# Optimization experiments

Hardware: AMD Instinct MI355X
Metric: run time of the kernel (lower is better)

Reference implementation:

```python
import jax, jax.numpy as jnp
import numpy as np

B, L, D = 8, 2048, 1024   # batch, seq_len, d_model
E, H, K = 8, 512, 2       # num_experts, expert_hidden, top_k
LN_EPS = 1e-5


def setup_inputs() -> dict:
    key = jax.random.key(0)
    ks = jax.random.split(key, 4)
    rn = lambda k, shape, sc: (jax.random.normal(k, shape, jnp.float32) * sc)
    return {
        "x": rn(ks[0], (B, L, D), 1.0),
        "ln_w": jnp.ones((D,), jnp.float32),
        "ln_b": jnp.zeros((D,), jnp.float32),
        "gate_w": rn(ks[1], (D, E), 0.02),
        "gate_b": jnp.zeros((E,), jnp.float32),
        "w1": rn(ks[2], (E, D, H), 0.02),
        "b1": jnp.zeros((E, H), jnp.float32),
        "w2": rn(ks[3], (E, H, D), 0.02),
        "b2": jnp.zeros((E, D), jnp.float32),
    }


def reference(x, ln_w, ln_b, gate_w, gate_b, w1, b1, w2, b2):
    Bx, Lx, Dx = x.shape
    xf = x.reshape(-1, Dx)                                   # [N, D]

    # gate = LayerNorm -> Linear (eval mode: no noise)
    mu = xf.mean(-1, keepdims=True)
    var = ((xf - mu) ** 2).mean(-1, keepdims=True)
    xn = (xf - mu) * jax.lax.rsqrt(var + LN_EPS) * ln_w + ln_b
    gate_logits = xn @ gate_w + gate_b                       # [N, E]
    gate_weights = jax.nn.softmax(gate_logits, axis=-1)      # [N, E]

    top_w, top_idx = jax.lax.top_k(gate_weights, K)          # [N, K]
    top_w = top_w / top_w.sum(-1, keepdims=True)

    # dense all-experts compute (faithful to the torch module)
    h = jax.nn.gelu(jnp.einsum('nd,edh->neh', xf, w1) + b1, approximate=False)  # [N, E, H]
    expert_out = jnp.einsum('neh,ehd->ned', h, w2) + b2      # [N, E, D]

    # gather selected experts and weighted-combine
    sel = jnp.take_along_axis(expert_out, top_idx[:, :, None], axis=1)  # [N, K, D]
    out = (top_w[:, :, None] * sel).sum(axis=1).reshape(Bx, Lx, Dx)
    return out, gate_weights
```

## Files before the change

kernel.cpp:

```cpp
#include <hip/hip_runtime.h>
#include <hip/hip_bf16.h>

#define N_TOK 16384
#define DM 1024
#define HD 512
#define NE 8
#define LN_EPS 1e-5f

typedef __attribute__((ext_vector_type(8))) short v8s;
typedef __attribute__((ext_vector_type(4))) float v4f;

__device__ __forceinline__ unsigned short f2bf(float f) {
  union { float f; unsigned u; } c; c.f = f;
  unsigned u = c.u + 0x7FFFu + ((c.u >> 16) & 1u);
  return (unsigned short)(u >> 16);
}

__device__ __forceinline__ float gelu_f(float v) {
  return 0.5f * v * (1.0f + erff(v * 0.7071067811865475f));
}

__global__ __launch_bounds__(256) void gate_kernel(
    const float* __restrict__ x, const float* __restrict__ lnw,
    const float* __restrict__ lnb, const float* __restrict__ gw,
    const float* __restrict__ gb, float* __restrict__ gates_out,
    int* __restrict__ ce, float* __restrict__ cw)
{
  const int wv = threadIdx.x >> 6, l = threadIdx.x & 63;
  const int n = blockIdx.x * 4 + wv;
  const float* xr = x + (size_t)n * DM;
  float4 v[4]; float s = 0.f, s2 = 0.f;
#pragma unroll
  for (int j = 0; j < 4; ++j) {
    v[j] = *(const float4*)(xr + l * 4 + j * 256);
    s  += v[j].x + v[j].y + v[j].z + v[j].w;
    s2 += v[j].x * v[j].x + v[j].y * v[j].y + v[j].z * v[j].z + v[j].w * v[j].w;
  }
#pragma unroll
  for (int m = 1; m < 64; m <<= 1) { s += __shfl_xor(s, m); s2 += __shfl_xor(s2, m); }
  const float mu = s * (1.f / DM);
  const float var = s2 * (1.f / DM) - mu * mu;
  const float rstd = 1.f / sqrtf(var + LN_EPS);
  float acc[8] = {0, 0, 0, 0, 0, 0, 0, 0};
#pragma unroll
  for (int j = 0; j < 4; ++j) {
#pragma unroll
    for (int q = 0; q < 4; ++q) {
      int d = l * 4 + j * 256 + q;
      float xv = (q == 0) ? v[j].x : (q == 1) ? v[j].y : (q == 2) ? v[j].z : v[j].w;
      float xn = (xv - mu) * rstd * lnw[d] + lnb[d];
      const float4 g0 = *(const float4*)(gw + d * 8);
      const float4 g1 = *(const float4*)(gw + d * 8 + 4);
      acc[0] += xn * g0.x; acc[1] += xn * g0.y; acc[2] += xn * g0.z; acc[3] += xn * g0.w;
      acc[4] += xn * g1.x; acc[5] += xn * g1.y; acc[6] += xn * g1.z; acc[7] += xn * g1.w;
    }
  }
#pragma unroll
  for (int e = 0; e < 8; ++e)
#pragma unroll
    for (int m = 1; m < 64; m <<= 1) acc[e] += __shfl_xor(acc[e], m);

  if (l == 0) {
    float lg[8], p[8], g[8];
    float mx = -1e30f;
    for (int e = 0; e < 8; ++e) { lg[e] = acc[e] + gb[e]; mx = fmaxf(mx, lg[e]); }
    float sum = 0.f;
    for (int e = 0; e < 8; ++e) { p[e] = expf(lg[e] - mx); sum += p[e]; }
    float inv = 1.f / sum;
    for (int e = 0; e < 8; ++e) g[e] = p[e] * inv;
    float4* go = (float4*)(gates_out + (size_t)n * 8);
    go[0] = make_float4(g[0], g[1], g[2], g[3]);
    go[1] = make_float4(g[4], g[5], g[6], g[7]);
    int e0 = 0; float b0 = g[0];
    for (int e = 1; e < 8; ++e) if (g[e] > b0) { b0 = g[e]; e0 = e; }
    int e1 = -1; float b1v = -1.f;
    for (int e = 0; e < 8; ++e) if (e != e0 && g[e] > b1v) { b1v = g[e]; e1 = e; }
    float wsum = b0 + b1v;
    ce[2 * n] = e0; ce[2 * n + 1] = e1;
    cw[2 * n] = b0 / wsum; cw[2 * n + 1] = b1v / wsum;
  }
}

__global__ __launch_bounds__(256) void route_kernel(
    const int* __restrict__ ce, const float* __restrict__ cw,
    int* __restrict__ counts, int* __restrict__ tids, float* __restrict__ pws)
{
  __shared__ int cnt;
  const int e = blockIdx.x;
  if (threadIdx.x == 0) cnt = 0;
  __syncthreads();
  for (int i = threadIdx.x; i < 2 * N_TOK; i += 256) {
    if (ce[i] == e) {
      int p = atomicAdd(&cnt, 1);
      tids[e * N_TOK + p] = i >> 1;
      pws[e * N_TOK + p] = cw[i];
    }
  }
  __syncthreads();
  if (threadIdx.x == 0) counts[e] = cnt;
}

__global__ __launch_bounds__(256) void transpose_cvt(
    const float* __restrict__ in, unsigned short* __restrict__ out, int R, int C)
{
  __shared__ float tile[64][65];
  const int tilesC = C >> 6, tilesR = R >> 6;
  const int perE = tilesR * tilesC;
  int bt = blockIdx.x;
  const int e = bt / perE; int rem = bt - e * perE;
  const int tr = rem / tilesC, tc = rem - tr * tilesC;
  const float* ip = in + (size_t)e * R * C;
  unsigned short* op = out + (size_t)e * R * C;
  const int r0 = tr * 64, c0 = tc * 64;
#pragma unroll
  for (int i = 0; i < 16; ++i) {
    int idx = i * 256 + threadIdx.x;
    int rr = idx >> 6, cc = idx & 63;
    tile[rr][cc] = ip[(size_t)(r0 + rr) * C + (c0 + cc)];
  }
  __syncthreads();
#pragma unroll
  for (int i = 0; i < 16; ++i) {
    int idx = i * 256 + threadIdx.x;
    int rr = idx >> 6, cc = idx & 63;
    op[(size_t)(c0 + rr) * R + (r0 + cc)] = f2bf(tile[cc][rr]);
  }
}

#define H_OFF   0
#define XS_OFF  65536
#define W1S_OFF 73728
#define W2S_OFF 65536
#define TOK_OFF 139264
#define WT_OFF  139520
#define SMEM_BYTES 139776

template<bool FULL>
__global__ __launch_bounds__(512, 2) void ffn_kernel(
    const float* __restrict__ x,
    const float* __restrict__ w1, const float* __restrict__ b1,
    const float* __restrict__ w2, const float* __restrict__ b2,
    const unsigned short* __restrict__ w1t, const unsigned short* __restrict__ w2t,
    const int* __restrict__ counts, const int* __restrict__ tids,
    const float* __restrict__ pws, float* __restrict__ outp)
{
  extern __shared__ char smem[];
  const int e = blockIdx.x & 7;
  const int tile = blockIdx.x >> 3;
  const int cnt = counts[e];
  const int base = tile * 64;
  if (base >= cnt) return;
  const int t = threadIdx.x;
  const int w = t >> 6, l = t & 63;
  const int lrow = l & 15, lhi = l >> 4;

  int* tokL = (int*)(smem + TOK_OFF);
  float* wtL = (float*)(smem + WT_OFF);
  if (t < 64) {
    int i = base + t;
    bool ok = i < cnt;
    int src = e * N_TOK + (ok ? i : base);
    tokL[t] = tids[src];
    wtL[t] = ok ? pws[src] : 0.f;
  }
  __syncthreads();

  v4f acc[4][4];
#pragma unroll
  for (int a = 0; a < 4; ++a)
#pragma unroll
    for (int b = 0; b < 4; ++b) acc[a][b] = (v4f){0.f, 0.f, 0.f, 0.f};

  for (int kt = 0; kt < 16; ++kt) {
    const int k0 = kt * 64;
    {
      const int tokr = t >> 3, ks = t & 7;
      const float* src = x + (size_t)tokL[tokr] * DM + k0 + ks * 8;
      float f[8];
      *(float4*)(f) = *(const float4*)src;
      *(float4*)(f + 4) = *(const float4*)(src + 4);
      v8s pv;
#pragma unroll
      for (int j = 0; j < 8; ++j) pv[j] = (short)f2bf(f[j]);
      *(v8s*)(smem + XS_OFF + tokr * 128 + ((ks ^ (tokr & 7)) << 4)) = pv;
    }
    if (FULL) {
#pragma unroll
      for (int i = 0; i < 8; ++i) {
        int c = i * 512 + t;
        int h = c >> 3, ks = c & 7;
        v8s val = *(const v8s*)(w1t + ((size_t)e * HD + h) * DM + k0 + ks * 8);
        *(v8s*)(smem + W1S_OFF + h * 128 + ((ks ^ (h & 7)) << 4)) = val;
      }
    } else {
      const int h = t;
#pragma unroll
      for (int i = 0; i < 8; ++i) {
        float f[8];
#pragma unroll
        for (int j = 0; j < 8; ++j) f[j] = w1[((size_t)e * DM + k0 + i * 8 + j) * HD + h];
        v8s pv;
#pragma unroll
        for (int j = 0; j < 8; ++j) pv[j] = (short)f2bf(f[j]);
        *(v8s*)(smem + W1S_OFF + h * 128 + ((i ^ (h & 7)) << 4)) = pv;
      }
    }
    __syncthreads();
#pragma unroll
    for (int ks2 = 0; ks2 < 2; ++ks2) {
      const int sb = (ks2 << 2) + lhi;
      v8s af[4], bfr[4];
#pragma unroll
      for (int mi = 0; mi < 4; ++mi) {
        int row = mi * 16 + lrow;
        af[mi] = *(const v8s*)(smem + XS_OFF + row * 128 + ((sb ^ (row & 7)) << 4));
      }
#pragma unroll
      for (int nj = 0; nj < 4; ++nj) {
        int col = (w << 6) + nj * 16 + lrow;
        bfr[nj] = *(const v8s*)(smem + W1S_OFF + col * 128 + ((sb ^ (col & 7)) << 4));
      }
#pragma unroll
      for (int mi = 0; mi < 4; ++mi)
#pragma unroll
        for (int nj = 0; nj < 4; ++nj)
          acc[mi][nj] = __builtin_amdgcn_mfma_f32_16x16x32_bf16(af[mi], bfr[nj], acc[mi][nj], 0, 0, 0);
    }
    __syncthreads();
  }

#pragma unroll
  for (int nj = 0; nj < 4; ++nj) {
    const int col = (w << 6) + nj * 16 + lrow;
    const float b1v = b1[e * HD + col];
#pragma unroll
    for (int mi = 0; mi < 4; ++mi) {
#pragma unroll
      for (int r = 0; r < 4; ++r) {
        int row = mi * 16 + lhi * 4 + r;
        float g = gelu_f(acc[mi][nj][r] + b1v);
        *(unsigned short*)(smem + H_OFF + row * 1024 + ((col * 2) ^ ((row & 7) << 4))) = f2bf(g);
      }
    }
  }
  __syncthreads();

  for (int nc = 0; nc < 4; ++nc) {
    v4f acc2[4][2];
#pragma unroll
    for (int a = 0; a < 4; ++a)
#pragma unroll
      for (int b = 0; b < 2; ++b) acc2[a][b] = (v4f){0.f, 0.f, 0.f, 0.f};
    for (int k2 = 0; k2 < 8; ++k2) {
      const int h0 = k2 * 64;
      if (FULL) {
#pragma unroll
        for (int i = 0; i < 4; ++i) {
          int c = i * 512 + t;
          int dloc = c >> 3, ks = c & 7;
          v8s val = *(const v8s*)(w2t + ((size_t)e * DM + nc * 256 + dloc) * HD + h0 + ks * 8);
          *(v8s*)(smem + W2S_OFF + dloc * 128 + ((ks ^ (dloc & 7)) << 4)) = val;
        }
      } else {
        const int dloc = t & 255;
        const int kb = t >> 8;
#pragma unroll
        for (int i = 0; i < 4; ++i) {
          int ks = kb + i * 2;
          float f[8];
#pragma unroll
          for (int j = 0; j < 8; ++j) f[j] = w2[((size_t)e * HD + h0 + ks * 8 + j) * DM + nc * 256 + dloc];
          v8s pv;
#pragma unroll
          for (int j = 0; j < 8; ++j) pv[j] = (short)f2bf(f[j]);
          *(v8s*)(smem + W2S_OFF + dloc * 128 + ((ks ^ (dloc & 7)) << 4)) = pv;
        }
      }
      __syncthreads();
#pragma unroll
      for (int ks2 = 0; ks2 < 2; ++ks2) {
        const int sb = (ks2 << 2) + lhi;
        v8s af[4], bfr[2];
#pragma unroll
        for (int mi = 0; mi < 4; ++mi) {
          int row = mi * 16 + lrow;
          int slin = (h0 >> 3) + sb;
          af[mi] = *(const v8s*)(smem + H_OFF + row * 1024 + ((slin ^ (row & 7)) << 4));
        }
#pragma unroll
        for (int nj = 0; nj < 2; ++nj) {
          int dl = (w << 5) + nj * 16 + lrow;
          bfr[nj] = *(const v8s*)(smem + W2S_OFF + dl * 128 + ((sb ^ (dl & 7)) << 4));
        }
#pragma unroll
        for (int mi = 0; mi < 4; ++mi)
#pragma unroll
          for (int nj = 0; nj < 2; ++nj)
            acc2[mi][nj] = __builtin_amdgcn_mfma_f32_16x16x32_bf16(af[mi], bfr[nj], acc2[mi][nj], 0, 0, 0);
      }
      __syncthreads();
    }
#pragma unroll
    for (int nj = 0; nj < 2; ++nj) {
      const int dl = (w << 5) + nj * 16 + lrow;
      const int d = nc * 256 + dl;
      const float b2v = b2[e * DM + d];
#pragma unroll
      for (int mi = 0; mi < 4; ++mi) {
#pragma unroll
        for (int r = 0; r < 4; ++r) {
          int row = mi * 16 + lhi * 4 + r;
          float val = wtL[row] * (acc2[mi][nj][r] + b2v);
          atomicAdd(outp + (size_t)tokL[row] * DM + d, val);
        }
      }
    }
  }
}

extern "C" void kernel_launch(void* const* d_in, const int* in_sizes, int n_in,
                              void* d_out, int out_size, void* d_ws, size_t ws_size,
                              hipStream_t stream)
{
  const float* x   = (const float*)d_in[0];
  const float* lnw = (const float*)d_in[1];
  const float* lnb = (const float*)d_in[2];
  const float* gw  = (const float*)d_in[3];
  const float* gb  = (const float*)d_in[4];
  const float* w1  = (const float*)d_in[5];
  const float* b1  = (const float*)d_in[6];
  const float* w2  = (const float*)d_in[7];
  const float* b2  = (const float*)d_in[8];
  float* out = (float*)d_out;
  float* gates_out = out + (size_t)N_TOK * DM;

  char* ws = (char*)d_ws;
  int*   ce     = (int*)(ws + 0);
  float* cw     = (float*)(ws + 131072);
  int*   counts = (int*)(ws + 262144);
  int*   tids   = (int*)(ws + 262400);
  float* pws    = (float*)(ws + 786688);
  unsigned short* w1t = (unsigned short*)(ws + 1310976);
  unsigned short* w2t = (unsigned short*)(ws + 9699584);
  const bool full = ws_size >= 18088192ull;

  hipMemsetAsync(d_out, 0, (size_t)N_TOK * DM * sizeof(float), stream);
  gate_kernel<<<N_TOK / 4, 256, 0, stream>>>(x, lnw, lnb, gw, gb, gates_out, ce, cw);
  route_kernel<<<NE, 256, 0, stream>>>(ce, cw, counts, tids, pws);
  if (full) {
    transpose_cvt<<<NE * 16 * 8, 256, 0, stream>>>(w1, w1t, DM, HD);
    transpose_cvt<<<NE * 8 * 16, 256, 0, stream>>>(w2, w2t, HD, DM);
    hipFuncSetAttribute((const void*)&ffn_kernel<true>,
                        hipFuncAttributeMaxDynamicSharedMemorySize, SMEM_BYTES);
    ffn_kernel<true><<<NE * 256, 512, SMEM_BYTES, stream>>>(
        x, w1, b1, w2, b2, w1t, w2t, counts, tids, pws, out);
  } else {
    hipFuncSetAttribute((const void*)&ffn_kernel<false>,
                        hipFuncAttributeMaxDynamicSharedMemorySize, SMEM_BYTES);
    ffn_kernel<false><<<NE * 256, 512, SMEM_BYTES, stream>>>(
        x, w1, b1, w2, b2, w1t, w2t, counts, tids, pws, out);
  }
}
```

Measured before the change: 614.9 us.

## Split fused expert FFN into two grouped bf16 GEMMs with direct-to-LDS loads

When the workspace is large enough, the gate kernel also writes a bf16 copy of x. The fused per-expert FFN is replaced by two grouped GEMM kernels: gemm1 computes GELU(x W1 + b1) into a bf16 hidden buffer, and gemm2 multiplies by W2 and atomically accumulates the routing-weighted result into the output. Both use 128x128 tiles, swizzled LDS and global_load_lds transfers, and launch a fixed grid sized for the worst case, with surplus blocks exiting early. This targets better MFMA utilization and occupancy, at the cost of a hidden-state round trip through global memory, extra workspace, and fp32 atomics on the output.

```diff
diff --git a/kernel.cpp b/kernel.cpp
--- a/kernel.cpp
+++ b/kernel.cpp
@@ -6,9 +6,17 @@
 #define HD 512
 #define NE 8
 #define LN_EPS 1e-5f
+#define MT_MAX 264
 
 typedef __attribute__((ext_vector_type(8))) short v8s;
 typedef __attribute__((ext_vector_type(4))) float v4f;
+
+typedef const __attribute__((address_space(1))) unsigned int* as1cu;
+typedef __attribute__((address_space(3))) unsigned int* as3u;
+
+__device__ __forceinline__ void gl_lds16(const void* g, void* l) {
+  __builtin_amdgcn_global_load_lds((as1cu)g, (as3u)l, 16, 0, 0);
+}
 
 __device__ __forceinline__ unsigned short f2bf(float f) {
   union { float f; unsigned u; } c; c.f = f;
@@ -24,7 +32,8 @@
     const float* __restrict__ x, const float* __restrict__ lnw,
     const float* __restrict__ lnb, const float* __restrict__ gw,
     const float* __restrict__ gb, float* __restrict__ gates_out,
-    int* __restrict__ ce, float* __restrict__ cw)
+    int* __restrict__ ce, float* __restrict__ cw,
+    unsigned short* __restrict__ xbf)
 {
   const int wv = threadIdx.x >> 6, l = threadIdx.x & 63;
   const int n = blockIdx.x * 4 + wv;
@@ -35,6 +44,16 @@
     v[j] = *(const float4*)(xr + l * 4 + j * 256);
     s  += v[j].x + v[j].y + v[j].z + v[j].w;
     s2 += v[j].x * v[j].x + v[j].y * v[j].y + v[j].z * v[j].z + v[j].w * v[j].w;
+  }
+  if (xbf) {
+    unsigned long long* xbo = (unsigned long long*)(xbf + (size_t)n * DM);
+#pragma unroll
+    for (int j = 0; j < 4; ++j) {
+      union { unsigned short u[4]; unsigned long long ll; } pk;
+      pk.u[0] = f2bf(v[j].x); pk.u[1] = f2bf(v[j].y);
+      pk.u[2] = f2bf(v[j].z); pk.u[3] = f2bf(v[j].w);
+      xbo[l + j * 64] = pk.ll;
+    }
   }
 #pragma unroll
   for (int m = 1; m < 64; m <<= 1) { s += __shfl_xor(s, m); s2 += __shfl_xor(s2, m); }
@@ -127,6 +146,226 @@
   }
 }
 
+__global__ __launch_bounds__(256, 3) void gemm1_kernel(
+    const unsigned short* __restrict__ xbf, const unsigned short* __restrict__ w1t,
+    const float* __restrict__ b1,
+    const int* __restrict__ counts, const int* __restrict__ tids,
+    unsigned short* __restrict__ hbuf)
+{
+  __shared__ unsigned short As[128 * 64];
+  __shared__ unsigned short Bs[128 * 64];
+  __shared__ int tokL[128];
+  __shared__ int sE, sBase, sCnt;
+
+  const int t = threadIdx.x;
+  const int bid = blockIdx.x;
+  const int nt = bid / MT_MAX;
+  const int mt = bid - nt * MT_MAX;
+
+  if (t == 0) {
+    int pref = 0, e = -1, base = 0, cn = 0;
+    for (int i = 0; i < NE; ++i) {
+      int c = counts[i];
+      int tiles = (c + 127) >> 7;
+      if (mt < pref + tiles) { e = i; base = (mt - pref) << 7; cn = c; break; }
+      pref += tiles;
+    }
+    sE = e; sBase = base; sCnt = cn;
+  }
+  __syncthreads();
+  const int e = sE;
+  if (e < 0) return;
+  const int cnt = sCnt, baseI = sBase;
+
+  if (t < 128) {
+    int i = baseI + t;
+    tokL[t] = (i < cnt) ? tids[e * N_TOK + i] : tids[e * N_TOK];
+  }
+  __syncthreads();
+
+  const unsigned short* gA[4];
+  const unsigned short* gB[4];
+#pragma unroll
+  for (int i = 0; i < 4; ++i) {
+    int c = i * 256 + t;
+    int row = c >> 3, ks = c & 7;
+    int kswz = ks ^ (row & 7);
+    gA[i] = xbf + (size_t)tokL[row] * DM + kswz * 8;
+    gB[i] = w1t + ((size_t)e * HD + nt * 128 + row) * DM + kswz * 8;
+  }
+  const int w = t >> 6, l = t & 63;
+  const int wr = w >> 1, wc = w & 1;
+  const int lrow = l & 15, lhi = l >> 4;
+  char* AsB = (char*)As;
+  char* BsB = (char*)Bs;
+  char* ldsA = AsB + w * 1024;
+  char* ldsB = BsB + w * 1024;
+
+  v4f acc[4][4];
+#pragma unroll
+  for (int a = 0; a < 4; ++a)
+#pragma unroll
+    for (int b = 0; b < 4; ++b) acc[a][b] = (v4f){0.f, 0.f, 0.f, 0.f};
+
+  for (int kt = 0; kt < 16; ++kt) {
+    __syncthreads();
+#pragma unroll
+    for (int i = 0; i < 4; ++i) {
+      gl_lds16(gA[i] + kt * 64, ldsA + i * 4096);
+      gl_lds16(gB[i] + kt * 64, ldsB + i * 4096);
+    }
+    __syncthreads();
+#pragma unroll
+    for (int ks2 = 0; ks2 < 2; ++ks2) {
+      const int sb = ks2 * 4 + lhi;
+      v8s a[4], b[4];
+#pragma unroll
+      for (int mi = 0; mi < 4; ++mi) {
+        int row = wr * 64 + mi * 16 + lrow;
+        a[mi] = *(const v8s*)(AsB + row * 128 + ((sb ^ (row & 7)) << 4));
+      }
+#pragma unroll
+      for (int nj = 0; nj < 4; ++nj) {
+        int col = wc * 64 + nj * 16 + lrow;
+        b[nj] = *(const v8s*)(BsB + col * 128 + ((sb ^ (col & 7)) << 4));
+      }
+#pragma unroll
+      for (int mi = 0; mi < 4; ++mi)
+#pragma unroll
+        for (int nj = 0; nj < 4; ++nj)
+          acc[mi][nj] = __builtin_amdgcn_mfma_f32_16x16x32_bf16(a[mi], b[nj], acc[mi][nj], 0, 0, 0);
+    }
+  }
+
+#pragma unroll
+  for (int nj = 0; nj < 4; ++nj) {
+    const int col = nt * 128 + wc * 64 + nj * 16 + lrow;
+    const float bb = b1[e * HD + col];
+#pragma unroll
+    for (int mi = 0; mi < 4; ++mi) {
+      const int row0 = wr * 64 + mi * 16 + lhi * 4;
+#pragma unroll
+      for (int r = 0; r < 4; ++r) {
+        float g = gelu_f(acc[mi][nj][r] + bb);
+        hbuf[(size_t)(mt * 128 + row0 + r) * HD + col] = f2bf(g);
+      }
+    }
+  }
+}
+
+__global__ __launch_bounds__(256, 3) void gemm2_kernel(
+    const unsigned short* __restrict__ hbuf, const unsigned short* __restrict__ w2t,
+    const float* __restrict__ b2,
+    const int* __restrict__ counts, const int* __restrict__ tids,
+    const float* __restrict__ pws, float* __restrict__ outp)
+{
+  __shared__ unsigned short As[128 * 64];
+  __shared__ unsigned short Bs[128 * 64];
+  __shared__ int tokL[128];
+  __shared__ float wtL[128];
+  __shared__ int sE, sBase, sCnt;
+
+  const int t = threadIdx.x;
+  const int bid = blockIdx.x;
+  const int nt = bid / MT_MAX;
+  const int mt = bid - nt * MT_MAX;
+
+  if (t == 0) {
+    int pref = 0, e = -1, base = 0, cn = 0;
+    for (int i = 0; i < NE; ++i) {
+      int c = counts[i];
+      int tiles = (c + 127) >> 7;
+      if (mt < pref + tiles) { e = i; base = (mt - pref) << 7; cn = c; break; }
+      pref += tiles;
+    }
+    sE = e; sBase = base; sCnt = cn;
+  }
+  __syncthreads();
+  const int e = sE;
+  if (e < 0) return;
+  const int cnt = sCnt, baseI = sBase;
+
+  if (t < 128) {
+    int i = baseI + t;
+    bool ok = i < cnt;
+    tokL[t] = ok ? tids[e * N_TOK + i] : 0;
+    wtL[t] = ok ? pws[e * N_TOK + i] : 0.f;
+  }
+  __syncthreads();
+
+  const unsigned short* gA[4];
+  const unsigned short* gB[4];
+#pragma unroll
+  for (int i = 0; i < 4; ++i) {
+    int c = i * 256 + t;
+    int row = c >> 3, ks = c & 7;
+    int kswz = ks ^ (row & 7);
+    gA[i] = hbuf + (size_t)(mt * 128 + row) * HD + kswz * 8;
+    gB[i] = w2t + ((size_t)e * DM + nt * 128 + row) * HD + kswz * 8;
+  }
+  const int w = t >> 6, l = t & 63;
+  const int wr = w >> 1, wc = w & 1;
+  const int lrow = l & 15, lhi = l >> 4;
+  char* AsB = (char*)As;
+  char* BsB = (char*)Bs;
+  char* ldsA = AsB + w * 1024;
+  char* ldsB = BsB + w * 1024;
+
+  v4f acc[4][4];
+#pragma unroll
+  for (int a = 0; a < 4; ++a)
+#pragma unroll
+    for (int b = 0; b < 4; ++b) acc[a][b] = (v4f){0.f, 0.f, 0.f, 0.f};
+
+  for (int kt = 0; kt < 8; ++kt) {
+    __syncthreads();
+#pragma unroll
+    for (int i = 0; i < 4; ++i) {
+      gl_lds16(gA[i] + kt * 64, ldsA + i * 4096);
+      gl_lds16(gB[i] + kt * 64, ldsB + i * 4096);
+    }
+    __syncthreads();
+#pragma unroll
+    for (int ks2 = 0; ks2 < 2; ++ks2) {
+      const int sb = ks2 * 4 + lhi;
+      v8s a[4], b[4];
+#pragma unroll
+      for (int mi = 0; mi < 4; ++mi) {
+        int row = wr * 64 + mi * 16 + lrow;
+        a[mi] = *(const v8s*)(AsB + row * 128 + ((sb ^ (row & 7)) << 4));
+      }
+#pragma unroll
+      for (int nj = 0; nj < 4; ++nj) {
+        int col = wc * 64 + nj * 16 + lrow;
+        b[nj] = *(const v8s*)(BsB + col * 128 + ((sb ^ (col & 7)) << 4));
+      }
+#pragma unroll
+      for (int mi = 0; mi < 4; ++mi)
+#pragma unroll
+        for (int nj = 0; nj < 4; ++nj)
+          acc[mi][nj] = __builtin_amdgcn_mfma_f32_16x16x32_bf16(a[mi], b[nj], acc[mi][nj], 0, 0, 0);
+    }
+  }
+
+#pragma unroll
+  for (int nj = 0; nj < 4; ++nj) {
+    const int col = nt * 128 + wc * 64 + nj * 16 + lrow;
+    const float bb = b2[e * DM + col];
+#pragma unroll
+    for (int mi = 0; mi < 4; ++mi) {
+      const int rbase = wr * 64 + mi * 16 + lhi * 4;
+#pragma unroll
+      for (int r = 0; r < 4; ++r) {
+        const int rloc = rbase + r;
+        if (baseI + rloc < cnt) {
+          float val = wtL[rloc] * (acc[mi][nj][r] + bb);
+          atomicAdd(outp + (size_t)tokL[rloc] * DM + col, val);
+        }
+      }
+    }
+  }
+}
+
 #define H_OFF   0
 #define XS_OFF  65536
 #define W1S_OFF 73728
@@ -342,22 +581,35 @@
   float* pws    = (float*)(ws + 786688);
   unsigned short* w1t = (unsigned short*)(ws + 1310976);
   unsigned short* w2t = (unsigned short*)(ws + 9699584);
-  const bool full = ws_size >= 18088192ull;
+  unsigned short* xbf = (unsigned short*)(ws + 18088192);
+  unsigned short* hbuf = (unsigned short*)(ws + 51642624);
+  const size_t NEED_NEW = 86245632ull;
+  const size_t NEED_FULL = 18088192ull;
 
   hipMemsetAsync(d_out, 0, (size_t)N_TOK * DM * sizeof(float), stream);
-  gate_kernel<<<N_TOK / 4, 256, 0, stream>>>(x, lnw, lnb, gw, gb, gates_out, ce, cw);
-  route_kernel<<<NE, 256, 0, stream>>>(ce, cw, counts, tids, pws);
-  if (full) {
+
+  if (ws_size >= NEED_NEW) {
+    gate_kernel<<<N_TOK / 4, 256, 0, stream>>>(x, lnw, lnb, gw, gb, gates_out, ce, cw, xbf);
+    route_kernel<<<NE, 256, 0, stream>>>(ce, cw, counts, tids, pws);
     transpose_cvt<<<NE * 16 * 8, 256, 0, stream>>>(w1, w1t, DM, HD);
     transpose_cvt<<<NE * 8 * 16, 256, 0, stream>>>(w2, w2t, HD, DM);
-    hipFuncSetAttribute((const void*)&ffn_kernel<true>,
-                        hipFuncAttributeMaxDynamicSharedMemorySize, SMEM_BYTES);
-    ffn_kernel<true><<<NE * 256, 512, SMEM_BYTES, stream>>>(
-        x, w1, b1, w2, b2, w1t, w2t, counts, tids, pws, out);
+    gemm1_kernel<<<4 * MT_MAX, 256, 0, stream>>>(xbf, w1t, b1, counts, tids, hbuf);
+    gemm2_kernel<<<8 * MT_MAX, 256, 0, stream>>>(hbuf, w2t, b2, counts, tids, pws, out);
   } else {
-    hipFuncSetAttribute((const void*)&ffn_kernel<false>,
-                        hipFuncAttributeMaxDynamicSharedMemorySize, SMEM_BYTES);
-    ffn_kernel<false><<<NE * 256, 512, SMEM_BYTES, stream>>>(
-        x, w1, b1, w2, b2, w1t, w2t, counts, tids, pws, out);
-  }
-}
+    gate_kernel<<<N_TOK / 4, 256, 0, stream>>>(x, lnw, lnb, gw, gb, gates_out, ce, cw, nullptr);
+    route_kernel<<<NE, 256, 0, stream>>>(ce, cw, counts, tids, pws);
+    if (ws_size >= NEED_FULL) {
+      transpose_cvt<<<NE * 16 * 8, 256, 0, stream>>>(w1, w1t, DM, HD);
+      transpose_cvt<<<NE * 8 * 16, 256, 0, stream>>>(w2, w2t, HD, DM);
+      hipFuncSetAttribute((const void*)&ffn_kernel<true>,
+                          hipFuncAttributeMaxDynamicSharedMemorySize, SMEM_BYTES);
+      ffn_kernel<true><<<NE * 256, 512, SMEM_BYTES, stream>>>(
+          x, w1, b1, w2, b2, w1t, w2t, counts, tids, pws, out);
+    } else {
+      hipFuncSetAttribute((const void*)&ffn_kernel<false>,
+                          hipFuncAttributeMaxDynamicSharedMemorySize, SMEM_BYTES);
+      ffn_kernel<false><<<NE * 256, 512, SMEM_BYTES, stream>>>(
+          x, w1, b1, w2, b2, w1t, w2t, counts, tids, pws, out);
+    }
+  }
+}
```

Result: faster. 506.8 us (-17.6%).
